# Kernel tuning notes

Measured on AMD Instinct MI355X. Metric: run time of the kernel, lower is better.

The kernel has to match this reference:

```python
import jax, jax.numpy as jnp
import numpy as np

NA, NKPT, NC = 3, 17, 1
NO_DET = NC + 5              # 6
NO = NO_DET + 3 * NKPT       # 57
ANCHORS = np.array([[19,27,44,40,38,94],[96,68,86,152,180,137],[140,301,303,264,238,542]], dtype=np.float32).reshape(3, 3, 2)
STRIDES = np.array([8.0, 16.0, 32.0], dtype=np.float32)
CH = (256, 512, 1024)
HW = (80, 40, 20)
B = 16


def setup_inputs():
    key = jax.random.key(0)
    ks = jax.random.split(key, 18)
    d = {}
    ki = 0
    for i, (c, hw) in enumerate(zip(CH, HW)):
        d[f"f{i}"] = jax.random.normal(ks[ki], (B, c, hw, hw), jnp.float32); ki += 1
        d[f"ia{i}"] = jax.random.normal(ks[ki], (1, c, 1, 1), jnp.float32) * 0.02; ki += 1
        d[f"w{i}"] = jax.random.normal(ks[ki], (NA * NO_DET, c), jnp.float32) * (1.0 / np.sqrt(c)); ki += 1
        d[f"b{i}"] = jnp.zeros((NA * NO_DET,), jnp.float32)
        d[f"im{i}"] = 1.0 + jax.random.normal(ks[ki], (1, NA * NO_DET, 1, 1), jnp.float32) * 0.02; ki += 1
        d[f"wk{i}"] = jax.random.normal(ks[ki], (NA * 3 * NKPT, c), jnp.float32) * (1.0 / np.sqrt(c)); ki += 1
        d[f"bk{i}"] = jnp.zeros((NA * 3 * NKPT,), jnp.float32)
    return d


def _decode(feat, ia, w, b, im, wk, bk, anchors_l, stride):
    # ImplicitA -> 1x1 conv -> ImplicitM (det branch); plain 1x1 conv (kpt branch)
    det = jnp.einsum('bchw,oc->bohw', feat + ia, w) + b[None, :, None, None]
    det = det * im
    kpt = jnp.einsum('bchw,oc->bohw', feat, wk) + bk[None, :, None, None]
    x = jnp.concatenate([det, kpt], axis=1)          # (B, na*no, H, W)
    Bb, _, H, W = x.shape
    x = x.reshape(Bb, NA, NO, H, W).transpose(0, 1, 3, 4, 2)  # (B, na, H, W, no)
    yv, xv = jnp.meshgrid(jnp.arange(H), jnp.arange(W), indexing='ij')
    grid = jnp.stack([xv, yv], -1).astype(x.dtype)[None, None]  # (1,1,H,W,2)
    xd = jax.nn.sigmoid(x[..., :NO_DET])
    xy = (xd[..., 0:2] * 2.0 - 0.5 + grid) * stride
    wh = (xd[..., 2:4] * 2.0) ** 2 * anchors_l.reshape(1, NA, 1, 1, 2)
    kp = x[..., NO_DET:]                              # (B, na, H, W, 51)
    kx = (kp[..., 0::3] * 2.0 - 0.5 + grid[..., 0:1]) * stride
    ky = (kp[..., 1::3] * 2.0 - 0.5 + grid[..., 1:2]) * stride
    kc = jax.nn.sigmoid(kp[..., 2::3])
    kdec = jnp.stack([kx, ky, kc], -1).reshape(Bb, NA, H, W, 3 * NKPT)
    y = jnp.concatenate([xy, wh, xd[..., 4:], kdec], -1)  # (B, na, H, W, 57)
    return y.reshape(Bb, -1, NO)


def reference(f0, ia0, w0, b0, im0, wk0, bk0,
              f1, ia1, w1, b1, im1, wk1, bk1,
              f2, ia2, w2, b2, im2, wk2, bk2):
    anchors = jnp.asarray(ANCHORS)
    z0 = _decode(f0, ia0, w0, b0, im0, wk0, bk0, anchors[0], STRIDES[0])
    z1 = _decode(f1, ia1, w1, b1, im1, wk1, bk1, anchors[1], STRIDES[1])
    z2 = _decode(f2, ia2, w2, b2, im2, wk2, bk2, anchors[2], STRIDES[2])
    return jnp.concatenate([z0, z1, z2], axis=1)      # (B, 25200, 57)
```

## Files before the change

### kernel.cpp

```cpp
#include <hip/hip_runtime.h>
#include <hip/hip_bf16.h>

typedef __attribute__((ext_vector_type(8))) short short8;
typedef __attribute__((ext_vector_type(4))) float floatx4;

__device__ __forceinline__ float sigm(float x) { return 1.0f / (1.0f + __expf(-x)); }

__device__ __forceinline__ unsigned short f2bf(float v) {
  union { __hip_bfloat16 h; unsigned short u; } cv;
  cv.h = __float2bfloat16(v);
  return cv.u;
}

struct PrepArgs {
  const float *w, *b, *im, *ia, *wk, *bk;
  unsigned short* Wp;
  float* bias;
  int C;
};

__global__ void prep_kernel(PrepArgs A0, PrepArgs A1, PrepArgs A2) {
  PrepArgs A = (blockIdx.y == 0) ? A0 : (blockIdx.y == 1) ? A1 : A2;
  const int n = blockIdx.x;
  const int t = threadIdx.x;
  const int C = A.C;
  unsigned short* wrow = A.Wp + (size_t)n * C;
  if (n >= 171) {
    for (int k = t; k < C; k += 64) wrow[k] = 0;
    if (t == 0) A.bias[n] = 0.0f;
    return;
  }
  if (n < 18) {
    const float* src = A.w + (size_t)n * C;
    const float sc = A.im[n];
    float dot = 0.0f;
    for (int k = t; k < C; k += 64) {
      float v = src[k];
      dot += v * A.ia[k];
      wrow[k] = f2bf(v * sc);
    }
#pragma unroll
    for (int off = 32; off > 0; off >>= 1) dot += __shfl_down(dot, off);
    if (t == 0) A.bias[n] = sc * (A.b[n] + dot);
  } else {
    const float* src = A.wk + (size_t)(n - 18) * C;
    for (int k = t; k < C; k += 64) wrow[k] = f2bf(src[k]);
    if (t == 0) A.bias[n] = A.bk[n - 18];
  }
}

#define LDS_BYTES 36864

template <int SC, int C, int HW, int W>
__device__ __forceinline__ void gemm_decode(const float* __restrict__ feat,
                                            const unsigned short* __restrict__ Wp,
                                            const float* __restrict__ bias,
                                            float* __restrict__ out, int tile, char* smem) {
  constexpr float STRD = (SC == 0) ? 8.0f : (SC == 1) ? 16.0f : 32.0f;
  constexpr int ZOFF = (SC == 0) ? 0 : (SC == 1) ? 19200 : 24000;
  constexpr int I = C / 64;

  const int t = threadIdx.x;
  const int lane = t & 63;
  const int wv = t >> 6;
  const int l15 = lane & 15;
  const int quad = lane >> 4;

  unsigned short* Alds = (unsigned short*)smem;
  float* Elds = (float*)smem;

  const int r = lane & 31;
  const int kh = lane >> 5;
  const int mG = tile * 128 + wv * 32 + r;
  const int bA = mG / HW;
  const int pA = mG - bA * HW;
  const float* gL = feat + ((size_t)bA * C + kh * 32) * (size_t)HW + pA;

  floatx4 acc[2][11];
#pragma unroll
  for (int mi = 0; mi < 2; ++mi)
#pragma unroll
    for (int nj = 0; nj < 11; ++nj) acc[mi][nj] = (floatx4){0.f, 0.f, 0.f, 0.f};

  const unsigned short* bP = Wp + (size_t)l15 * C + quad * 8;
  unsigned short* wD = Alds + wv * 4608 + r * 72 + kh * 32;
  const unsigned short* aB = Alds + wv * 4608 + l15 * 72 + quad * 8;

  float v[32];
  auto loadA = [&](int it) {
    const float* g = gL + (size_t)it * 64 * HW;
#pragma unroll
    for (int kk = 0; kk < 32; ++kk) v[kk] = g[(size_t)kk * HW];
  };
  auto writeA = [&](int pb) {
    unsigned short* d = wD + pb * 2304;
#pragma unroll
    for (int c8 = 0; c8 < 4; ++c8) {
      short8 s;
#pragma unroll
      for (int j = 0; j < 8; ++j) s[j] = (short)f2bf(v[c8 * 8 + j]);
      *(short8*)(d + c8 * 8) = s;
    }
  };
  auto mfmaStep = [&](int it) {
    const int pb = it & 1;
    const unsigned short* a = aB + pb * 2304;
    short8 af[2][2];
#pragma unroll
    for (int mi = 0; mi < 2; ++mi)
#pragma unroll
      for (int h = 0; h < 2; ++h) af[mi][h] = *(const short8*)(a + mi * 1152 + h * 32);
    const unsigned short* bI = bP + it * 64;
#pragma unroll
    for (int nj = 0; nj < 11; ++nj) {
      short8 b0 = *(const short8*)(bI + (size_t)nj * 16 * C);
      short8 b1 = *(const short8*)(bI + (size_t)nj * 16 * C + 32);
      acc[0][nj] = __builtin_amdgcn_mfma_f32_16x16x32_bf16(af[0][0], b0, acc[0][nj], 0, 0, 0);
      acc[1][nj] = __builtin_amdgcn_mfma_f32_16x16x32_bf16(af[1][0], b0, acc[1][nj], 0, 0, 0);
      acc[0][nj] = __builtin_amdgcn_mfma_f32_16x16x32_bf16(af[0][1], b1, acc[0][nj], 0, 0, 0);
      acc[1][nj] = __builtin_amdgcn_mfma_f32_16x16x32_bf16(af[1][1], b1, acc[1][nj], 0, 0, 0);
    }
  };

  loadA(0);
#pragma unroll
  for (int it = 0; it < I - 1; ++it) {
    writeA(it & 1);
    loadA(it + 1);
    mfmaStep(it);
  }
  writeA((I - 1) & 1);
  mfmaStep(I - 1);

  float bj[11];
#pragma unroll
  for (int nj = 0; nj < 11; ++nj) bj[nj] = bias[nj * 16 + l15];

#pragma unroll
  for (int c = 0; c < 4; ++c) {
    __syncthreads();
    if (wv == c) {
#pragma unroll
      for (int nj = 0; nj < 11; ++nj)
#pragma unroll
        for (int mi = 0; mi < 2; ++mi)
#pragma unroll
          for (int rr = 0; rr < 4; ++rr)
            Elds[(mi * 16 + quad * 4 + rr) * 180 + nj * 16 + l15] = acc[mi][nj][rr] + bj[nj];
    }
    __syncthreads();
    if (t < 192) {
      const int task = t >> 1, half = t & 1;
      const int row = task & 31, a = task >> 5;
      const int m = tile * 128 + c * 32 + row;
      const int bb = m / HW;
      const int p = m - bb * HW;
      const float fx = (float)(p % W);
      const float fy = (float)(p / W);
      float* L = Elds + row * 180 + a * 57;
      if (half == 0) {
        float aw, ah;
        if constexpr (SC == 0) {
          aw = (a == 0) ? 19.f : (a == 1) ? 44.f : 38.f;
          ah = (a == 0) ? 27.f : (a == 1) ? 40.f : 94.f;
        } else if constexpr (SC == 1) {
          aw = (a == 0) ? 96.f : (a == 1) ? 86.f : 180.f;
          ah = (a == 0) ? 68.f : (a == 1) ? 152.f : 137.f;
        } else {
          aw = (a == 0) ? 140.f : (a == 1) ? 303.f : 238.f;
          ah = (a == 0) ? 301.f : (a == 1) ? 264.f : 542.f;
        }
        float r0 = L[0], r1 = L[1], r2 = L[2], r3 = L[3], r4 = L[4], r5 = L[5];
        L[0] = (sigm(r0) * 2.f - 0.5f + fx) * STRD;
        L[1] = (sigm(r1) * 2.f - 0.5f + fy) * STRD;
        float tw = sigm(r2) * 2.f;
        L[2] = tw * tw * aw;
        float th = sigm(r3) * 2.f;
        L[3] = th * th * ah;
        L[4] = sigm(r4);
        L[5] = sigm(r5);
#pragma unroll
        for (int kp = 0; kp < 8; ++kp) {
          float kx = L[6 + 3 * kp], ky = L[7 + 3 * kp], kc = L[8 + 3 * kp];
          L[6 + 3 * kp] = (kx * 2.f - 0.5f + fx) * STRD;
          L[7 + 3 * kp] = (ky * 2.f - 0.5f + fy) * STRD;
          L[8 + 3 * kp] = sigm(kc);
        }
      } else {
#pragma unroll
        for (int kp = 8; kp < 17; ++kp) {
          float kx = L[6 + 3 * kp], ky = L[7 + 3 * kp], kc = L[8 + 3 * kp];
          L[6 + 3 * kp] = (kx * 2.f - 0.5f + fx) * STRD;
          L[7 + 3 * kp] = (ky * 2.f - 0.5f + fy) * STRD;
          L[8 + 3 * kp] = sigm(kc);
        }
      }
    }
    __syncthreads();
    for (int i = t; i < 96 * 57; i += 256) {
      int sr = i / 57;
      int j = i - sr * 57;
      int a = sr >> 5, row = sr & 31;
      int m = tile * 128 + c * 32 + row;
      int bb = m / HW;
      int p = m - bb * HW;
      out[((size_t)bb * 25200 + (size_t)(ZOFF + a * HW + p)) * 57 + j] =
          Elds[row * 180 + a * 57 + j];
    }
  }
}

__global__ __launch_bounds__(256, 2) void main_kernel(
    const float* __restrict__ f0, const float* __restrict__ f1, const float* __restrict__ f2,
    const unsigned short* __restrict__ Wp0, const unsigned short* __restrict__ Wp1,
    const unsigned short* __restrict__ Wp2, const float* __restrict__ b0,
    const float* __restrict__ b1, const float* __restrict__ b2, float* __restrict__ out) {
  __shared__ __align__(16) char smem[LDS_BYTES];
  const int bid = blockIdx.x;
  if (bid < 50)
    gemm_decode<2, 1024, 400, 20>(f2, Wp2, b2, out, bid, smem);
  else if (bid < 250)
    gemm_decode<1, 512, 1600, 40>(f1, Wp1, b1, out, bid - 50, smem);
  else
    gemm_decode<0, 256, 6400, 80>(f0, Wp0, b0, out, bid - 250, smem);
}

extern "C" void kernel_launch(void* const* d_in, const int* in_sizes, int n_in, void* d_out,
                              int out_size, void* d_ws, size_t ws_size, hipStream_t stream) {
  const float *f[3], *ia[3], *w[3], *b[3], *im[3], *wk[3], *bk[3];
  for (int s = 0; s < 3; ++s) {
    f[s] = (const float*)d_in[7 * s + 0];
    ia[s] = (const float*)d_in[7 * s + 1];
    w[s] = (const float*)d_in[7 * s + 2];
    b[s] = (const float*)d_in[7 * s + 3];
    im[s] = (const float*)d_in[7 * s + 4];
    wk[s] = (const float*)d_in[7 * s + 5];
    bk[s] = (const float*)d_in[7 * s + 6];
  }
  char* ws = (char*)d_ws;
  unsigned short* Wp0 = (unsigned short*)(ws + 0);
  unsigned short* Wp1 = (unsigned short*)(ws + 90112);
  unsigned short* Wp2 = (unsigned short*)(ws + 270336);
  float* bias0 = (float*)(ws + 630784);
  float* bias1 = (float*)(ws + 631488);
  float* bias2 = (float*)(ws + 632192);

  PrepArgs A0 = {w[0], b[0], im[0], ia[0], wk[0], bk[0], Wp0, bias0, 256};
  PrepArgs A1 = {w[1], b[1], im[1], ia[1], wk[1], bk[1], Wp1, bias1, 512};
  PrepArgs A2 = {w[2], b[2], im[2], ia[2], wk[2], bk[2], Wp2, bias2, 1024};
  prep_kernel<<<dim3(176, 3), 64, 0, stream>>>(A0, A1, A2);

  main_kernel<<<1050, 256, 0, stream>>>(f[0], f[1], f[2], Wp0, Wp1, Wp2, bias0, bias1, bias2,
                                        (float*)d_out);
}
```

Measured before the change: 341.7 us.

## Halve M tile, stage weights in LDS via global_load_lds, raise occupancy

Each block now covers 64 pixel rows instead of 128. The four waves split the K dimension for loading activations, and each wave computes one 16-row M slice across all output columns. Weight tiles are loaded straight into swizzled LDS with global_load_lds instead of each wave reading them from global memory, and the grid doubles with launch bounds raised to 4 blocks per CU. The goal is less per-wave weight traffic and fewer registers, so more blocks fit per CU and latency is better hidden. In exchange the activation buffer loses double buffering, each K step needs two barriers, and the weight padding grows to 192 rows.

```diff
diff --git a/kernel.cpp b/kernel.cpp
--- a/kernel.cpp
+++ b/kernel.cpp
@@ -10,6 +10,11 @@
   union { __hip_bfloat16 h; unsigned short u; } cv;
   cv.h = __float2bfloat16(v);
   return cv.u;
+}
+
+__device__ __forceinline__ void glds16(const void* g, void* l) {
+  __builtin_amdgcn_global_load_lds((const __attribute__((address_space(1))) void*)g,
+                                   (__attribute__((address_space(3))) void*)l, 16, 0, 0);
 }
 
 struct PrepArgs {
@@ -49,7 +54,7 @@
   }
 }
 
-#define LDS_BYTES 36864
+#define LDS_BYTES 34560
 
 template <int SC, int C, int HW, int W>
 __device__ __forceinline__ void gemm_decode(const float* __restrict__ feat,
@@ -67,92 +72,89 @@
   const int quad = lane >> 4;
 
   unsigned short* Alds = (unsigned short*)smem;
+  char* BB = smem + 9216;
   float* Elds = (float*)smem;
 
-  const int r = lane & 31;
-  const int kh = lane >> 5;
-  const int mG = tile * 128 + wv * 32 + r;
-  const int bA = mG / HW;
-  const int pA = mG - bA * HW;
-  const float* gL = feat + ((size_t)bA * C + kh * 32) * (size_t)HW + pA;
-
-  floatx4 acc[2][11];
-#pragma unroll
-  for (int mi = 0; mi < 2; ++mi)
-#pragma unroll
-    for (int nj = 0; nj < 11; ++nj) acc[mi][nj] = (floatx4){0.f, 0.f, 0.f, 0.f};
-
-  const unsigned short* bP = Wp + (size_t)l15 * C + quad * 8;
-  unsigned short* wD = Alds + wv * 4608 + r * 72 + kh * 32;
-  const unsigned short* aB = Alds + wv * 4608 + l15 * 72 + quad * 8;
-
-  float v[32];
+  const int mA = tile * 64 + lane;
+  const int bA = mA / HW;
+  const int pA = mA - bA * HW;
+  const float* fbase = feat + ((size_t)bA * C + wv * 16) * (size_t)HW + pA;
+
+  const int rsub = lane >> 3;
+  const int csw = (lane & 7) ^ rsub;
+  const char* WpB = (const char*)Wp;
+
+  floatx4 acc[11];
+#pragma unroll
+  for (int nj = 0; nj < 11; ++nj) acc[nj] = (floatx4){0.f, 0.f, 0.f, 0.f};
+
+  const unsigned short* aRd = Alds + (wv * 16 + l15) * 72 + quad * 8;
+  const int c0 = quad ^ (l15 & 7);
+  const char* bRd0 = BB + (size_t)l15 * 128 + c0 * 16;
+  const char* bRd1 = BB + (size_t)l15 * 128 + (c0 ^ 4) * 16;
+
+  float v[16];
   auto loadA = [&](int it) {
-    const float* g = gL + (size_t)it * 64 * HW;
-#pragma unroll
-    for (int kk = 0; kk < 32; ++kk) v[kk] = g[(size_t)kk * HW];
+    const float* g = fbase + (size_t)it * 64 * HW;
+#pragma unroll
+    for (int kk = 0; kk < 16; ++kk) v[kk] = g[(size_t)kk * HW];
   };
-  auto writeA = [&](int pb) {
-    unsigned short* d = wD + pb * 2304;
-#pragma unroll
-    for (int c8 = 0; c8 < 4; ++c8) {
-      short8 s;
-#pragma unroll
-      for (int j = 0; j < 8; ++j) s[j] = (short)f2bf(v[c8 * 8 + j]);
-      *(short8*)(d + c8 * 8) = s;
-    }
+  auto writeA = [&]() {
+    short8 s0, s1;
+#pragma unroll
+    for (int j = 0; j < 8; ++j) {
+      s0[j] = (short)f2bf(v[j]);
+      s1[j] = (short)f2bf(v[j + 8]);
+    }
+    *(short8*)(Alds + lane * 72 + wv * 16) = s0;
+    *(short8*)(Alds + lane * 72 + wv * 16 + 8) = s1;
   };
-  auto mfmaStep = [&](int it) {
-    const int pb = it & 1;
-    const unsigned short* a = aB + pb * 2304;
-    short8 af[2][2];
-#pragma unroll
-    for (int mi = 0; mi < 2; ++mi)
-#pragma unroll
-      for (int h = 0; h < 2; ++h) af[mi][h] = *(const short8*)(a + mi * 1152 + h * 32);
-    const unsigned short* bI = bP + it * 64;
+
+  loadA(0);
+  for (int it = 0; it < I; ++it) {
+    asm volatile("s_barrier" ::: "memory");
+#pragma unroll
+    for (int j = 0; j < 6; ++j) {
+      const int rowb = wv * 48 + j * 8;
+      const void* gsrc = WpB + ((size_t)(rowb + rsub) * C + (size_t)it * 64) * 2 + csw * 16;
+      glds16(gsrc, BB + rowb * 128);
+    }
+    __builtin_amdgcn_sched_barrier(0);
+    writeA();
+    loadA((it + 1 < I) ? it + 1 : it);
+    __builtin_amdgcn_sched_barrier(0);
+    asm volatile("s_waitcnt vmcnt(16) lgkmcnt(0)\n\ts_barrier" ::: "memory");
+    short8 af0 = *(const short8*)(aRd);
+    short8 af1 = *(const short8*)(aRd + 32);
 #pragma unroll
     for (int nj = 0; nj < 11; ++nj) {
-      short8 b0 = *(const short8*)(bI + (size_t)nj * 16 * C);
-      short8 b1 = *(const short8*)(bI + (size_t)nj * 16 * C + 32);
-      acc[0][nj] = __builtin_amdgcn_mfma_f32_16x16x32_bf16(af[0][0], b0, acc[0][nj], 0, 0, 0);
-      acc[1][nj] = __builtin_amdgcn_mfma_f32_16x16x32_bf16(af[1][0], b0, acc[1][nj], 0, 0, 0);
-      acc[0][nj] = __builtin_amdgcn_mfma_f32_16x16x32_bf16(af[0][1], b1, acc[0][nj], 0, 0, 0);
-      acc[1][nj] = __builtin_amdgcn_mfma_f32_16x16x32_bf16(af[1][1], b1, acc[1][nj], 0, 0, 0);
-    }
-  };
-
-  loadA(0);
-#pragma unroll
-  for (int it = 0; it < I - 1; ++it) {
-    writeA(it & 1);
-    loadA(it + 1);
-    mfmaStep(it);
-  }
-  writeA((I - 1) & 1);
-  mfmaStep(I - 1);
+      short8 b0 = *(const short8*)(bRd0 + (size_t)nj * 2048);
+      short8 b1 = *(const short8*)(bRd1 + (size_t)nj * 2048);
+      acc[nj] = __builtin_amdgcn_mfma_f32_16x16x32_bf16(af0, b0, acc[nj], 0, 0, 0);
+      acc[nj] = __builtin_amdgcn_mfma_f32_16x16x32_bf16(af1, b1, acc[nj], 0, 0, 0);
+    }
+  }
 
   float bj[11];
 #pragma unroll
   for (int nj = 0; nj < 11; ++nj) bj[nj] = bias[nj * 16 + l15];
 
 #pragma unroll
-  for (int c = 0; c < 4; ++c) {
+  for (int c = 0; c < 2; ++c) {
     __syncthreads();
-    if (wv == c) {
+    if ((wv >> 1) == c) {
+      const int rbase = (wv & 1) * 16 + quad * 4;
 #pragma unroll
       for (int nj = 0; nj < 11; ++nj)
 #pragma unroll
-        for (int mi = 0; mi < 2; ++mi)
-#pragma unroll
-          for (int rr = 0; rr < 4; ++rr)
-            Elds[(mi * 16 + quad * 4 + rr) * 180 + nj * 16 + l15] = acc[mi][nj][rr] + bj[nj];
+        for (int r = 0; r < 4; ++r)
+          Elds[(rbase + r) * 180 + nj * 16 + l15] = acc[nj][r] + bj[nj];
     }
     __syncthreads();
     if (t < 192) {
       const int task = t >> 1, half = t & 1;
       const int row = task & 31, a = task >> 5;
-      const int m = tile * 128 + c * 32 + row;
+      const int m = tile * 64 + c * 32 + row;
       const int bb = m / HW;
       const int p = m - bb * HW;
       const float fx = (float)(p % W);
@@ -201,7 +203,7 @@
       int sr = i / 57;
       int j = i - sr * 57;
       int a = sr >> 5, row = sr & 31;
-      int m = tile * 128 + c * 32 + row;
+      int m = tile * 64 + c * 32 + row;
       int bb = m / HW;
       int p = m - bb * HW;
       out[((size_t)bb * 25200 + (size_t)(ZOFF + a * HW + p)) * 57 + j] =
@@ -210,19 +212,19 @@
   }
 }
 
-__global__ __launch_bounds__(256, 2) void main_kernel(
+__global__ __launch_bounds__(256, 4) void main_kernel(
     const float* __restrict__ f0, const float* __restrict__ f1, const float* __restrict__ f2,
     const unsigned short* __restrict__ Wp0, const unsigned short* __restrict__ Wp1,
     const unsigned short* __restrict__ Wp2, const float* __restrict__ b0,
     const float* __restrict__ b1, const float* __restrict__ b2, float* __restrict__ out) {
   __shared__ __align__(16) char smem[LDS_BYTES];
   const int bid = blockIdx.x;
-  if (bid < 50)
+  if (bid < 100)
     gemm_decode<2, 1024, 400, 20>(f2, Wp2, b2, out, bid, smem);
-  else if (bid < 250)
-    gemm_decode<1, 512, 1600, 40>(f1, Wp1, b1, out, bid - 50, smem);
+  else if (bid < 500)
+    gemm_decode<1, 512, 1600, 40>(f1, Wp1, b1, out, bid - 100, smem);
   else
-    gemm_decode<0, 256, 6400, 80>(f0, Wp0, b0, out, bid - 250, smem);
+    gemm_decode<0, 256, 6400, 80>(f0, Wp0, b0, out, bid - 500, smem);
 }
 
 extern "C" void kernel_launch(void* const* d_in, const int* in_sizes, int n_in, void* d_out,
@@ -239,17 +241,17 @@
   }
   char* ws = (char*)d_ws;
   unsigned short* Wp0 = (unsigned short*)(ws + 0);
-  unsigned short* Wp1 = (unsigned short*)(ws + 90112);
-  unsigned short* Wp2 = (unsigned short*)(ws + 270336);
-  float* bias0 = (float*)(ws + 630784);
-  float* bias1 = (float*)(ws + 631488);
-  float* bias2 = (float*)(ws + 632192);
+  unsigned short* Wp1 = (unsigned short*)(ws + 98304);
+  unsigned short* Wp2 = (unsigned short*)(ws + 294912);
+  float* bias0 = (float*)(ws + 688128);
+  float* bias1 = (float*)(ws + 688896);
+  float* bias2 = (float*)(ws + 689664);
 
   PrepArgs A0 = {w[0], b[0], im[0], ia[0], wk[0], bk[0], Wp0, bias0, 256};
   PrepArgs A1 = {w[1], b[1], im[1], ia[1], wk[1], bk[1], Wp1, bias1, 512};
   PrepArgs A2 = {w[2], b[2], im[2], ia[2], wk[2], bk[2], Wp2, bias2, 1024};
-  prep_kernel<<<dim3(176, 3), 64, 0, stream>>>(A0, A1, A2);
-
-  main_kernel<<<1050, 256, 0, stream>>>(f[0], f[1], f[2], Wp0, Wp1, Wp2, bias0, bias1, bias2,
+  prep_kernel<<<dim3(192, 3), 64, 0, stream>>>(A0, A1, A2);
+
+  main_kernel<<<2100, 256, 0, stream>>>(f[0], f[1], f[2], Wp0, Wp1, Wp2, bias0, bias1, bias2,
                                         (float*)d_out);
 }
```

After: 297.0 us. 13.1% less time.
